# Optimization experiments

Measured on AMD Instinct MI355X. Metric: run time of the kernel, lower is better.

## Reference

```python
import jax, jax.numpy as jnp
import numpy as np

N = 50000   # nodes
E = 800000  # edges
G = 256     # graphs in batch
NF, EF, H, L = 16, 8, 128, 4
EPS = 1e-5


def setup_inputs() -> dict:
    key = jax.random.key(0)
    ks = jax.random.split(key, 20)
    s = 0.05
    return {
        "x": jax.random.normal(ks[0], (N, NF), jnp.float32),
        "edge_index": jax.random.randint(ks[1], (2, E), 0, N, dtype=jnp.int32),
        "edge_attr": jax.random.uniform(ks[2], (E, EF), jnp.float32),
        "batch": jnp.sort(jax.random.randint(ks[3], (N,), 0, G, dtype=jnp.int32)),
        "W_emb": jax.random.normal(ks[4], (NF, H), jnp.float32) * s,
        "b_emb": jnp.zeros((H,), jnp.float32),
        "Wf": jax.random.normal(ks[5], (L, 2 * H + EF, H), jnp.float32) * s,
        "bf": jnp.zeros((L, H), jnp.float32),
        "Ws": jax.random.normal(ks[6], (L, 2 * H + EF, H), jnp.float32) * s,
        "bs": jnp.zeros((L, H), jnp.float32),
        "gamma": jnp.ones((L, H), jnp.float32),
        "beta": jnp.zeros((L, H), jnp.float32),
        "W1": jax.random.normal(ks[7], (H, 64), jnp.float32) * s,
        "b1": jnp.zeros((64,), jnp.float32),
        "W2": jax.random.normal(ks[8], (64, 32), jnp.float32) * s,
        "b2": jnp.zeros((32,), jnp.float32),
        "W_out": jax.random.normal(ks[9], (32, 1), jnp.float32) * s,
        "b_out": jnp.zeros((1,), jnp.float32),
    }


def reference(x, edge_index, edge_attr, batch, W_emb, b_emb, Wf, bf, Ws, bs,
              gamma, beta, W1, b1, W2, b2, W_out, b_out):
    src, dst = edge_index[0], edge_index[1]  # message j->i: x_j=h[src], x_i=h[dst]
    h = jax.nn.relu(x @ W_emb + b_emb)       # [N, H]
    for l in range(L):
        # CGConv: z_ij = [x_i, x_j, e_ij]; gated message; sum-aggregate; +x residual
        z = jnp.concatenate([h[dst], h[src], edge_attr], axis=-1)  # [E, 2H+EF]
        m = jax.nn.sigmoid(z @ Wf[l] + bf[l]) * jax.nn.softplus(z @ Ws[l] + bs[l])
        agg = jax.ops.segment_sum(m, dst, num_segments=N)
        x_new = agg + h
        # BatchNorm1d (training-mode batch statistics, biased var)
        mu = x_new.mean(axis=0)
        var = x_new.var(axis=0)
        x_new = gamma[l] * (x_new - mu) * jax.lax.rsqrt(var + EPS) + beta[l]
        x_new = jax.nn.relu(x_new)
        h = h + x_new
    # global mean pool over graphs
    cnt = jax.ops.segment_sum(jnp.ones((N,), h.dtype), batch, num_segments=G)
    pooled = jax.ops.segment_sum(h, batch, num_segments=G) / jnp.maximum(cnt, 1.0)[:, None]
    g = jax.nn.relu(pooled @ W1 + b1)
    g = jax.nn.relu(g @ W2 + b2)
    return (g @ W_out + b_out).squeeze(-1)  # [G]
```

## Files before the change

### kernel.cpp

```cpp
#include <hip/hip_runtime.h>
#include <hip/hip_bf16.h>

#define H 128
#define EFD 8
#define NLAYER 4
#define ZDIM (2*H+EFD)

typedef float f32x2 __attribute__((ext_vector_type(2)));
typedef float f32x4 __attribute__((ext_vector_type(4)));
typedef short s16x8 __attribute__((ext_vector_type(8)));
typedef _Float16 f16x4 __attribute__((ext_vector_type(4)));
typedef unsigned int u32x2 __attribute__((ext_vector_type(2)));

#define PKFMA_LO(acc, a, b) asm("v_pk_fma_f32 %0, %1, %2, %0 op_sel:[0,0,0] op_sel_hi:[0,1,1]" : "+v"(acc) : "v"(a), "v"(b))
#define PKFMA_HI(acc, a, b) asm("v_pk_fma_f32 %0, %1, %2, %0 op_sel:[1,0,0] op_sel_hi:[1,1,1]" : "+v"(acc) : "v"(a), "v"(b))
#define PKFMA_LO_INIT(dst, a, b, c) asm("v_pk_fma_f32 %0, %1, %2, %3 op_sel:[0,0,0] op_sel_hi:[0,1,1]" : "=v"(dst) : "v"(a), "v"(b), "v"(c))
#define FMAMIX_LO(dst, h2, add) asm("v_fma_mix_f32 %0, %1, 1.0, %2 op_sel:[0,0,0] op_sel_hi:[1,0,0]" : "=v"(dst) : "v"(h2), "v"(add))
#define FMAMIX_HI(dst, h2, add) asm("v_fma_mix_f32 %0, %1, 1.0, %2 op_sel:[1,0,0] op_sel_hi:[1,0,0]" : "=v"(dst) : "v"(h2), "v"(add))

#define L2E 1.44269504088896340736f
#define LN2 0.69314718055994530942f

__device__ __forceinline__ unsigned short f2bf(float x){
    unsigned u = __float_as_uint(x);
    return (unsigned short)((u + 0x7FFFu + ((u>>16)&1u)) >> 16);
}

__global__ void embed_kernel(const float* __restrict__ x, const float* __restrict__ We,
                             const float* __restrict__ be, float* __restrict__ h, int N){
    int idx = blockIdx.x*blockDim.x + threadIdx.x;
    if (idx >= N*H) return;
    int n = idx >> 7, f = idx & 127;
    float a = be[f];
    #pragma unroll
    for (int k=0;k<16;k++) a = fmaf(x[n*16+k], We[k*H+f], a);
    h[idx] = fmaxf(a, 0.f);
}

__global__ void hist_kernel(const int* __restrict__ dstI, int* __restrict__ counts, int E){
    int e = blockIdx.x*blockDim.x + threadIdx.x;
    if (e < E) atomicAdd(&counts[dstI[e]], 1);
}

__global__ __launch_bounds__(1024) void scan1(const int* __restrict__ counts, int* __restrict__ incl,
                                              int* __restrict__ bsums, int N){
    __shared__ int lds[1024];
    int t = threadIdx.x;
    int i = blockIdx.x*1024 + t;
    int v = (i < N) ? counts[i] : 0;
    lds[t] = v;
    __syncthreads();
    for (int off=1; off<1024; off<<=1){
        int add = (t>=off) ? lds[t-off] : 0;
        __syncthreads();
        lds[t] += add;
        __syncthreads();
    }
    if (i < N) incl[i] = lds[t];
    if (t == 1023) bsums[blockIdx.x] = lds[1023];
}

__global__ __launch_bounds__(64) void scan2(int* bsums, int nb){
    int t = threadIdx.x;
    if (nb <= 64){
        int orig = (t < nb) ? bsums[t] : 0;
        int v = orig;
        for (int off=1; off<64; off<<=1){
            int n = __shfl_up(v, off);
            if (t >= off) v += n;
        }
        if (t < nb) bsums[t] = v - orig;
    } else if (t == 0){
        int run = 0;
        for (int b=0;b<nb;b++){ int v = bsums[b]; bsums[b] = run; run += v; }
    }
}

__global__ __launch_bounds__(1024) void scan3(const int* incl, const int* __restrict__ counts,
                                              const int* __restrict__ bsums, int* __restrict__ rowptr,
                                              int* cursor, int N, int E){
    int i = blockIdx.x*1024 + threadIdx.x;
    if (i >= N) return;
    int ex = incl[i] - counts[i] + bsums[blockIdx.x];
    rowptr[i] = ex;
    cursor[i] = ex;
    if (i == N-1) rowptr[N] = E;
}

__global__ void scatter_kernel(const int* __restrict__ srcI, const int* __restrict__ dstI,
                               const float* __restrict__ eattr, int* __restrict__ cursor,
                               int* __restrict__ src_s, float* __restrict__ ea_s, int E){
    int e = blockIdx.x*blockDim.x + threadIdx.x;
    if (e >= E) return;
    int d = dstI[e];
    int pos = atomicAdd(&cursor[d], 1);
    src_s[pos] = srcI[e];
    const float4* s4 = (const float4*)(eattr + (size_t)e*EFD);
    float4* o4 = (float4*)(ea_s + (size_t)pos*EFD);
    o4[0] = s4[0]; o4[1] = s4[1];
}

__global__ __launch_bounds__(256) void wpack_kernel(const float* __restrict__ Wf, const float* __restrict__ Ws,
        s16x8* __restrict__ bhi, s16x8* __restrict__ blo){
    int idx = blockIdx.x*256 + threadIdx.x;
    int l = idx & 63, ct = (idx>>6)&7, ks = (idx>>9)&3, w = (idx>>11)&3, layer = idx>>13;
    int cp = w*128 + ct*16 + (l&15);
    int k0 = ks*32 + ((l>>4)<<3);
    const float* WfL = Wf + (size_t)layer*ZDIM*H;
    const float* WsL = Ws + (size_t)layer*ZDIM*H;
    int colIn = cp & 127;
    int sel = cp >> 7;
    const float* Wm = (sel & 1) ? WsL : WfL;
    int krow = (sel >> 1) ? H : 0;
    s16x8 vh, vl;
    #pragma unroll
    for (int e=0;e<8;e++){
        float v = Wm[(size_t)(krow + k0 + e)*H + colIn];
        unsigned short hb = f2bf(v);
        float rem = v - __uint_as_float(((unsigned)hb)<<16);
        vh[e] = (short)hb;
        vl[e] = (short)f2bf(rem);
    }
    bhi[idx] = vh;
    blo[idx] = vl;
}

__global__ __launch_bounds__(512, 2) void table_mfma(
        float* __restrict__ h, const float* __restrict__ xn, const float* __restrict__ scsh,
        const s16x8* __restrict__ bhi, const s16x8* __restrict__ blo,
        const float* __restrict__ bf_l, const float* __restrict__ bs_l,
        float* __restrict__ TD, _Float16* __restrict__ TS16, int N, int layer, int ntiles){
    __shared__ __align__(16) short amat[2][32*136];
    const int t = threadIdx.x;
    const int lane = t & 63, W = t >> 6;
    const int ow = W >> 1, ctbase = (W & 1)*4;
    const int rbase = lane & 15, kg = lane >> 4;

    s16x8 Bh[4][4], Bl[4][4];
    {
        const size_t bbase = ((size_t)layer*4 + ow)*2048;
        #pragma unroll
        for (int ks=0;ks<4;ks++)
            #pragma unroll
            for (int c=0;c<4;c++){
                Bh[ks][c] = bhi[bbase + ks*512 + (ctbase+c)*64 + lane];
                Bl[ks][c] = blo[bbase + ks*512 + (ctbase+c)*64 + lane];
            }
        #pragma unroll
        for (int ks=0;ks<4;ks++)
            #pragma unroll
            for (int c=0;c<4;c++) asm volatile("" : "+v"(Bh[ks][c]), "+v"(Bl[ks][c]));
    }
    int c_local[4], off16[4];
    float bv[4];
    #pragma unroll
    for (int c=0;c<4;c++){
        c_local[c] = (ctbase+c)*16 + rbase;
        off16[c] = (c_local[c] >> 1)*4 + ((ow & 1) << 1) + (c_local[c] & 1);
        bv[c] = (ow == 0) ? bf_l[c_local[c]]*L2E : (ow == 1) ? bs_l[c_local[c]]*L2E : 0.f;
    }
    const int srow = t >> 4;
    const int kb = (t & 15)*8;
    float sc8[8], sh8[8];
    if (scsh){
        #pragma unroll
        for (int q=0;q<8;q+=4){
            *(float4*)&sc8[q] = *(const float4*)(scsh + kb + q);
            *(float4*)&sh8[q] = *(const float4*)(scsh + H + kb + q);
        }
    }

    for (int tile = blockIdx.x; tile < ntiles; tile += gridDim.x){
        const int n0 = tile*32;
        {
            const int gn = n0 + srow;
            const bool valid = gn < N;
            float* hr = h + (size_t)gn*H + kb;
            float vv[8];
            if (scsh){
                const float* xr = xn + (size_t)gn*H + kb;
                #pragma unroll
                for (int q=0;q<8;q+=4){
                    float4 xv = valid ? *(const float4*)(xr + q) : make_float4(0.f,0.f,0.f,0.f);
                    float4 hv = valid ? *(const float4*)(hr + q) : make_float4(0.f,0.f,0.f,0.f);
                    vv[q]   = hv.x + fmaxf(fmaf(xv.x, sc8[q],   sh8[q]),   0.f);
                    vv[q+1] = hv.y + fmaxf(fmaf(xv.y, sc8[q+1], sh8[q+1]), 0.f);
                    vv[q+2] = hv.z + fmaxf(fmaf(xv.z, sc8[q+2], sh8[q+2]), 0.f);
                    vv[q+3] = hv.w + fmaxf(fmaf(xv.w, sc8[q+3], sh8[q+3]), 0.f);
                }
                if (valid){
                    #pragma unroll
                    for (int q=0;q<8;q+=4){
                        float4 o; o.x=vv[q]; o.y=vv[q+1]; o.z=vv[q+2]; o.w=vv[q+3];
                        *(float4*)(hr + q) = o;
                    }
                }
            } else {
                #pragma unroll
                for (int q=0;q<8;q+=4){
                    float4 hv = valid ? *(const float4*)(hr + q) : make_float4(0.f,0.f,0.f,0.f);
                    vv[q]=hv.x; vv[q+1]=hv.y; vv[q+2]=hv.z; vv[q+3]=hv.w;
                }
            }
            s16x8 hv2, lv2;
            #pragma unroll
            for (int q=0;q<8;q++){
                unsigned short hb = f2bf(vv[q]);
                float rem = vv[q] - __uint_as_float(((unsigned)hb)<<16);
                hv2[q] = (short)hb;
                lv2[q] = (short)f2bf(rem);
            }
            *(s16x8*)&amat[0][srow*136 + kb] = hv2;
            *(s16x8*)&amat[1][srow*136 + kb] = lv2;
        }
        __syncthreads();
        f32x4 acc[2][4];
        #pragma unroll
        for (int rt=0;rt<2;rt++)
            #pragma unroll
            for (int c=0;c<4;c++){ acc[rt][c][0]=0.f; acc[rt][c][1]=0.f; acc[rt][c][2]=0.f; acc[rt][c][3]=0.f; }
        #pragma unroll
        for (int ks=0;ks<4;ks++){
            s16x8 ah[2], al[2];
            #pragma unroll
            for (int rt=0;rt<2;rt++){
                const int ao = (rbase + 16*rt)*136 + ks*32 + kg*8;
                ah[rt] = *(const s16x8*)&amat[0][ao];
                al[rt] = *(const s16x8*)&amat[1][ao];
            }
            #pragma unroll
            for (int c=0;c<4;c++)
                #pragma unroll
                for (int rt=0;rt<2;rt++){
                    acc[rt][c] = __builtin_amdgcn_mfma_f32_16x16x32_bf16(ah[rt], Bh[ks][c], acc[rt][c], 0, 0, 0);
                    acc[rt][c] = __builtin_amdgcn_mfma_f32_16x16x32_bf16(ah[rt], Bl[ks][c], acc[rt][c], 0, 0, 0);
                    acc[rt][c] = __builtin_amdgcn_mfma_f32_16x16x32_bf16(al[rt], Bh[ks][c], acc[rt][c], 0, 0, 0);
                }
        }
        if (ow < 2){
            const int colbase = (ow & 1)*128;
            #pragma unroll
            for (int c=0;c<4;c++)
                #pragma unroll
                for (int rt=0;rt<2;rt++){
                    const int nrow0 = n0 + 16*rt + kg*4;
                    #pragma unroll
                    for (int r=0;r<4;r++){
                        const int nd = nrow0 + r;
                        if (nd < N) TD[(size_t)nd*256 + colbase + c_local[c]] = fmaf(acc[rt][c][r], L2E, bv[c]);
                    }
                }
        } else {
            #pragma unroll
            for (int c=0;c<4;c++)
                #pragma unroll
                for (int rt=0;rt<2;rt++){
                    const int nrow0 = n0 + 16*rt + kg*4;
                    #pragma unroll
                    for (int r=0;r<4;r++){
                        const int nd = nrow0 + r;
                        if (nd < N) TS16[(size_t)nd*256 + off16[c]] = (_Float16)(acc[rt][c][r]*L2E);
                    }
                }
        }
        __syncthreads();
    }
}

__global__ __launch_bounds__(256, 4) void agg_kernel(
        const float* __restrict__ TD, const _Float16* __restrict__ TS16,
        const int* __restrict__ rowptr, const int* __restrict__ src_s, const float* __restrict__ ea_s,
        const float* __restrict__ Wf_l, const float* __restrict__ Ws_l,
        const float* __restrict__ h, float* __restrict__ xn, int N){
    __shared__ float wE[2048];
    const int t = threadIdx.x;
    {
        const float4* a = (const float4*)(Wf_l + 2*H*H);
        const float4* b = (const float4*)(Ws_l + 2*H*H);
        float4 va = a[t], vb = b[t];
        va.x*=L2E; va.y*=L2E; va.z*=L2E; va.w*=L2E;
        vb.x*=L2E; vb.y*=L2E; vb.z*=L2E; vb.w*=L2E;
        ((float4*)wE)[t] = va;
        ((float4*)wE)[256 + t] = vb;
    }
    __syncthreads();
    const int k = t & 63;
    const int i = blockIdx.x*4 + (t >> 6);
    if (i >= N) return;
    f32x2 wef2[8], wes2[8];
    #pragma unroll
    for (int r=0;r<8;r++){
        wef2[r] = *(const f32x2*)&wE[r*128 + 2*k];
        wes2[r] = *(const f32x2*)&wE[1024 + r*128 + 2*k];
    }
    #pragma unroll
    for (int r=0;r<8;r++) asm volatile("" : "+v"(wef2[r]), "+v"(wes2[r]));
    const f32x2* td = (const f32x2*)(TD + ((size_t)i << 8));
    f32x2 fd2 = td[k], sd2 = td[64+k];
    f32x2 acc = {0.f, 0.f};
    const int e0 = __builtin_amdgcn_readfirstlane(rowptr[i]);
    const int e1 = __builtin_amdgcn_readfirstlane(rowptr[i+1]);
    const int myoff = 4*k;
    const int last = e1 - 1;

    auto JID = [&](int e)->int {
        int ec = (e <= last) ? e : last;
        return __builtin_amdgcn_readfirstlane(src_s[ec]);
    };
    auto GATHER = [&](int j)->f16x4 {
        return *(const f16x4*)(TS16 + (((size_t)(unsigned)j) << 8) + myoff);
    };
    auto BODY = [&](int e, f16x4 tv){
        const float* ep = ea_s + (size_t)e*EFD;
        f32x4 eaA = *(const f32x4*)(ep);
        f32x4 eaB = *(const f32x4*)(ep + 4);
        f32x2 ea0 = __builtin_shufflevector(eaA, eaA, 0, 1);
        f32x2 ea1 = __builtin_shufflevector(eaA, eaA, 2, 3);
        f32x2 ea2 = __builtin_shufflevector(eaB, eaB, 0, 1);
        f32x2 ea3 = __builtin_shufflevector(eaB, eaB, 2, 3);
        f32x2 ef, es;
        PKFMA_LO_INIT(ef, ea0, wef2[0], fd2);
        PKFMA_HI(ef, ea0, wef2[1]);
        PKFMA_LO(ef, ea1, wef2[2]); PKFMA_HI(ef, ea1, wef2[3]);
        PKFMA_LO(ef, ea2, wef2[4]); PKFMA_HI(ef, ea2, wef2[5]);
        PKFMA_LO(ef, ea3, wef2[6]); PKFMA_HI(ef, ea3, wef2[7]);
        PKFMA_LO_INIT(es, ea0, wes2[0], sd2);
        PKFMA_HI(es, ea0, wes2[1]);
        PKFMA_LO(es, ea1, wes2[2]); PKFMA_HI(es, ea1, wes2[3]);
        PKFMA_LO(es, ea2, wes2[4]); PKFMA_HI(es, ea2, wes2[5]);
        PKFMA_LO(es, ea3, wes2[6]); PKFMA_HI(es, ea3, wes2[7]);
        u32x2 tu = *(u32x2*)&tv;
        float gx, gy, px, py;
        FMAMIX_LO(gx, tu.x, ef.x);
        FMAMIX_HI(gy, tu.x, ef.y);
        FMAMIX_LO(px, tu.y, es.x);
        FMAMIX_HI(py, tu.y, es.y);
        float sx = __builtin_amdgcn_rcpf(1.0f + __builtin_amdgcn_exp2f(-gx));
        float sy = __builtin_amdgcn_rcpf(1.0f + __builtin_amdgcn_exp2f(-gy));
        float tx = fmaxf(px, 0.f) + __builtin_amdgcn_logf(1.0f + __builtin_amdgcn_exp2f(-fabsf(px)));
        float ty = fmaxf(py, 0.f) + __builtin_amdgcn_logf(1.0f + __builtin_amdgcn_exp2f(-fabsf(py)));
        acc.x = fmaf(sx*tx, LN2, acc.x);
        acc.y = fmaf(sy*ty, LN2, acc.y);
    };

    if (e0 < e1){
        int j0 = JID(e0);
        int j1 = JID(e0+1);
        f16x4 tvA = GATHER(j0);
        f16x4 tvB = GATHER(j1);
        int jA = JID(e0+2);
        int jB = JID(e0+3);
        int e = e0;
        for (; e + 1 < e1; e += 2){
            int jA2 = JID(e+4);
            BODY(e, tvA);
            tvA = GATHER(jA);
            int jB2 = JID(e+5);
            BODY(e+1, tvB);
            tvB = GATHER(jB);
            jA = jA2; jB = jB2;
        }
        if (e < e1) BODY(e, tvA);
    }
    f32x2 hv = *(const f32x2*)(h + ((size_t)i << 7) + 2*k);
    f32x2 o = acc + hv;
    *(f32x2*)(xn + ((size_t)i << 7) + 2*k) = o;
}

__global__ __launch_bounds__(256) void stats_kernel(const float* __restrict__ xn, double* __restrict__ sums, int N){
    __shared__ double l1[128], l2[128];
    const int f = threadIdx.x & 127;
    const int half = threadIdx.x >> 7;
    const int nb = gridDim.x;
    const int per = (N + nb - 1)/nb;
    const int r0 = blockIdx.x*per;
    const int r1 = min(N, r0+per);
    double s = 0.0, s2 = 0.0;
    for (int r=r0+half; r<r1; r+=2){
        float v = xn[(size_t)r*H + f];
        s += v; s2 += (double)v*(double)v;
    }
    if (half == 1){ l1[f] = s; l2[f] = s2; }
    __syncthreads();
    if (half == 0){
        s += l1[f]; s2 += l2[f];
        atomicAdd(&sums[f], s);
        atomicAdd(&sums[H+f], s2);
    }
}

__global__ void finalize_bn(double* __restrict__ sums, const float* __restrict__ gamma_l,
                            const float* __restrict__ beta_l, float* __restrict__ scsh, int N){
    int f = threadIdx.x;
    if (f >= H) return;
    double mu = sums[f]/(double)N;
    double var = sums[H+f]/(double)N - mu*mu;
    if (var < 0.0) var = 0.0;
    float sc = (float)((double)gamma_l[f] / sqrt(var + 1e-5));
    scsh[f]   = sc;
    scsh[H+f] = (float)((double)beta_l[f] - mu*(double)sc);
    sums[f] = 0.0;
    sums[H+f] = 0.0;
}

__global__ __launch_bounds__(128) void pool_mlp_kernel(const float* __restrict__ h, const float* __restrict__ xn,
        const float* __restrict__ scsh, const int* __restrict__ batch,
        const float* __restrict__ W1, const float* __restrict__ b1,
        const float* __restrict__ W2, const float* __restrict__ b2,
        const float* __restrict__ Wo, const float* __restrict__ bo,
        float* __restrict__ out, int N){
    __shared__ float row[128];
    __shared__ float g1[64];
    __shared__ float g2[32];
    const int g = blockIdx.x;
    const int t = threadIdx.x;
    int lo = 0, hi = N;
    while (lo < hi){ int m = (lo+hi)>>1; if (batch[m] < g) lo = m+1; else hi = m; }
    const int s0 = lo;
    hi = N;
    while (lo < hi){ int m = (lo+hi)>>1; if (batch[m] < g+1) lo = m+1; else hi = m; }
    const int s1 = lo;
    const float sc = scsh[t], sh = scsh[H+t];
    float acc = 0.f;
    for (int r = s0; r < s1; ++r){
        float hv = h[(size_t)r*H + t];
        float xv = xn[(size_t)r*H + t];
        acc += hv + fmaxf(fmaf(xv, sc, sh), 0.f);
    }
    const float inv = 1.0f/fmaxf((float)(s1-s0), 1.0f);
    row[t] = acc*inv;
    __syncthreads();
    if (t < 64){
        float a = b1[t];
        #pragma unroll 4
        for (int i2=0;i2<128;i2++) a = fmaf(row[i2], W1[i2*64+t], a);
        g1[t] = fmaxf(a, 0.f);
    }
    __syncthreads();
    if (t < 32){
        float b = b2[t];
        #pragma unroll 4
        for (int i2=0;i2<64;i2++) b = fmaf(g1[i2], W2[i2*32+t], b);
        g2[t] = fmaxf(b, 0.f);
    }
    __syncthreads();
    if (t < 64){
        float p = (t < 32) ? g2[t]*Wo[t] : 0.f;
        for (int off=32; off>0; off>>=1) p += __shfl_down(p, off);
        if (t == 0) out[g] = p + bo[0];
    }
}

extern "C" void kernel_launch(void* const* d_in, const int* in_sizes, int n_in,
                              void* d_out, int out_size, void* d_ws, size_t ws_size,
                              hipStream_t stream){
    const float* x     = (const float*)d_in[0];
    const int*   eidx  = (const int*)d_in[1];
    const float* eattr = (const float*)d_in[2];
    const int*   batch = (const int*)d_in[3];
    const float* W_emb = (const float*)d_in[4];
    const float* b_emb = (const float*)d_in[5];
    const float* Wf    = (const float*)d_in[6];
    const float* bf    = (const float*)d_in[7];
    const float* Wsm   = (const float*)d_in[8];
    const float* bs    = (const float*)d_in[9];
    const float* gamma = (const float*)d_in[10];
    const float* beta  = (const float*)d_in[11];
    const float* W1    = (const float*)d_in[12];
    const float* b1    = (const float*)d_in[13];
    const float* W2    = (const float*)d_in[14];
    const float* b2    = (const float*)d_in[15];
    const float* Wo    = (const float*)d_in[16];
    const float* bo    = (const float*)d_in[17];
    float* out = (float*)d_out;

    const int N = in_sizes[0]/16;
    const int E = in_sizes[1]/2;
    const int G = out_size;

    const int* srcI = eidx;
    const int* dstI = eidx + E;

    char* p = (char*)d_ws;
    auto alloc = [&](size_t bytes)->char*{ char* r = p; p += (bytes + 255) & ~255ull; return r; };
    float*     h      = (float*)     alloc((size_t)N*H*4);
    float*     xn     = (float*)     alloc((size_t)N*H*4);
    float*     TD     = (float*)     alloc((size_t)N*2*H*4);
    _Float16*  TS16   = (_Float16*)  alloc((size_t)N*2*H*2);
    float*     ea_s   = (float*)     alloc((size_t)E*EFD*4);
    int*       src_s  = (int*)       alloc((size_t)E*4);
    int*       rowptr = (int*)       alloc((size_t)(N+1)*4);
    int*       cursor = (int*)       alloc((size_t)N*4);
    int*       counts = (int*)       alloc((size_t)N*4);
    int*       bsums  = (int*)       alloc(256*4);
    double*    sums   = (double*)    alloc(2*H*8);
    float*     scsh   = (float*)     alloc(2*H*4);
    s16x8*     bhi    = (s16x8*)     alloc((size_t)NLAYER*8192*16);
    s16x8*     blo    = (s16x8*)     alloc((size_t)NLAYER*8192*16);

    const int thr = 256;
    hipMemsetAsync(counts, 0, (size_t)N*4, stream);
    hipMemsetAsync(sums, 0, 2*H*8, stream);
    embed_kernel<<<(N*H + thr-1)/thr, thr, 0, stream>>>(x, W_emb, b_emb, h, N);
    hist_kernel<<<(E + thr-1)/thr, thr, 0, stream>>>(dstI, counts, E);
    int nb = (N + 1023)/1024;
    scan1<<<nb, 1024, 0, stream>>>(counts, cursor, bsums, N);
    scan2<<<1, 64, 0, stream>>>(bsums, nb);
    scan3<<<nb, 1024, 0, stream>>>(cursor, counts, bsums, rowptr, cursor, N, E);
    scatter_kernel<<<(E + thr-1)/thr, thr, 0, stream>>>(srcI, dstI, eattr, cursor, src_s, ea_s, E);
    wpack_kernel<<<128, 256, 0, stream>>>(Wf, Wsm, bhi, blo);

    const int ntiles = (N + 31)/32;
    for (int l=0;l<NLAYER;l++){
        table_mfma<<<256, 512, 0, stream>>>(h, xn, (l==0)?nullptr:scsh, bhi, blo,
                                            bf + l*H, bs + l*H, TD, TS16, N, l, ntiles);
        agg_kernel<<<(N+3)/4, 256, 0, stream>>>(TD, TS16, rowptr, src_s, ea_s,
                                                Wf + (size_t)l*ZDIM*H, Wsm + (size_t)l*ZDIM*H, h, xn, N);
        stats_kernel<<<256, 256, 0, stream>>>(xn, sums, N);
        finalize_bn<<<1, 128, 0, stream>>>(sums, gamma + l*H, beta + l*H, scsh, N);
    }

    pool_mlp_kernel<<<G, 128, 0, stream>>>(h, xn, scsh, batch, W1, b1, W2, b2, Wo, bo, out, N);
}
```

Measured before the change: 848.5 us.

## Merge dst/src tables into one fp16 row, stage outputs through LDS

The per-node destination table (previously fp32) and the source table (fp16) are combined into a single 512-half row per node, with the dst part also stored in fp16. table_mfma now writes MFMA results into a padded LDS tile and then emits coalesced 16-byte row stores, replacing scattered 2/4-byte global stores. This reduces table write traffic and store transaction count, and halves the dst-table read in agg. The cost is fp16 precision on the dst pre-activations, an extra LDS round trip and barrier, and larger LDS use that may limit occupancy.

```diff
diff --git a/kernel.cpp b/kernel.cpp
--- a/kernel.cpp
+++ b/kernel.cpp
@@ -20,6 +20,7 @@
 
 #define L2E 1.44269504088896340736f
 #define LN2 0.69314718055994530942f
+#define OPITCH 520
 
 __device__ __forceinline__ unsigned short f2bf(float x){
     unsigned u = __float_as_uint(x);
@@ -129,8 +130,9 @@
         float* __restrict__ h, const float* __restrict__ xn, const float* __restrict__ scsh,
         const s16x8* __restrict__ bhi, const s16x8* __restrict__ blo,
         const float* __restrict__ bf_l, const float* __restrict__ bs_l,
-        float* __restrict__ TD, _Float16* __restrict__ TS16, int N, int layer, int ntiles){
+        _Float16* __restrict__ T16, int N, int layer, int ntiles){
     __shared__ __align__(16) short amat[2][32*136];
+    __shared__ __align__(16) _Float16 outs[32*OPITCH];
     const int t = threadIdx.x;
     const int lane = t & 63, W = t >> 6;
     const int ow = W >> 1, ctbase = (W & 1)*4;
@@ -151,13 +153,13 @@
             #pragma unroll
             for (int c=0;c<4;c++) asm volatile("" : "+v"(Bh[ks][c]), "+v"(Bl[ks][c]));
     }
-    int c_local[4], off16[4];
+    int offT[4];
     float bv[4];
     #pragma unroll
     for (int c=0;c<4;c++){
-        c_local[c] = (ctbase+c)*16 + rbase;
-        off16[c] = (c_local[c] >> 1)*4 + ((ow & 1) << 1) + (c_local[c] & 1);
-        bv[c] = (ow == 0) ? bf_l[c_local[c]]*L2E : (ow == 1) ? bs_l[c_local[c]]*L2E : 0.f;
+        const int cl = (ctbase+c)*16 + rbase;
+        offT[c] = (ow>>1)*256 + ((cl>>1)<<2) + ((ow&1)<<1) + (cl&1);
+        bv[c] = (ow == 0) ? bf_l[cl]*L2E : (ow == 1) ? bs_l[cl]*L2E : 0.f;
     }
     const int srow = t >> 4;
     const int kb = (t & 15)*8;
@@ -237,38 +239,34 @@
                     acc[rt][c] = __builtin_amdgcn_mfma_f32_16x16x32_bf16(al[rt], Bh[ks][c], acc[rt][c], 0, 0, 0);
                 }
         }
-        if (ow < 2){
-            const int colbase = (ow & 1)*128;
-            #pragma unroll
-            for (int c=0;c<4;c++)
+        #pragma unroll
+        for (int c=0;c<4;c++)
+            #pragma unroll
+            for (int rt=0;rt<2;rt++){
+                const int nrow = 16*rt + kg*4;
                 #pragma unroll
-                for (int rt=0;rt<2;rt++){
-                    const int nrow0 = n0 + 16*rt + kg*4;
-                    #pragma unroll
-                    for (int r=0;r<4;r++){
-                        const int nd = nrow0 + r;
-                        if (nd < N) TD[(size_t)nd*256 + colbase + c_local[c]] = fmaf(acc[rt][c][r], L2E, bv[c]);
-                    }
+                for (int r=0;r<4;r++)
+                    outs[(nrow + r)*OPITCH + offT[c]] = (_Float16)fmaf(acc[rt][c][r], L2E, bv[c]);
+            }
+        __syncthreads();
+        {
+            const int colb = (t & 63)*8;
+            #pragma unroll
+            for (int ps=0; ps<4; ps++){
+                const int row = ps*8 + W;
+                const int nd = n0 + row;
+                if (nd < N){
+                    uint4 v = *(const uint4*)&outs[row*OPITCH + colb];
+                    *(uint4*)(T16 + (size_t)nd*512 + colb) = v;
                 }
-        } else {
-            #pragma unroll
-            for (int c=0;c<4;c++)
-                #pragma unroll
-                for (int rt=0;rt<2;rt++){
-                    const int nrow0 = n0 + 16*rt + kg*4;
-                    #pragma unroll
-                    for (int r=0;r<4;r++){
-                        const int nd = nrow0 + r;
-                        if (nd < N) TS16[(size_t)nd*256 + off16[c]] = (_Float16)(acc[rt][c][r]*L2E);
-                    }
-                }
+            }
         }
         __syncthreads();
     }
 }
 
 __global__ __launch_bounds__(256, 4) void agg_kernel(
-        const float* __restrict__ TD, const _Float16* __restrict__ TS16,
+        const _Float16* __restrict__ T16,
         const int* __restrict__ rowptr, const int* __restrict__ src_s, const float* __restrict__ ea_s,
         const float* __restrict__ Wf_l, const float* __restrict__ Ws_l,
         const float* __restrict__ h, float* __restrict__ xn, int N){
@@ -295,8 +293,10 @@
     }
     #pragma unroll
     for (int r=0;r<8;r++) asm volatile("" : "+v"(wef2[r]), "+v"(wes2[r]));
-    const f32x2* td = (const f32x2*)(TD + ((size_t)i << 8));
-    f32x2 fd2 = td[k], sd2 = td[64+k];
+    f16x4 dv = *(const f16x4*)(T16 + ((size_t)i << 9) + 4*k);
+    f32x2 fd2, sd2;
+    fd2.x = (float)dv[0]; fd2.y = (float)dv[1];
+    sd2.x = (float)dv[2]; sd2.y = (float)dv[3];
     f32x2 acc = {0.f, 0.f};
     const int e0 = __builtin_amdgcn_readfirstlane(rowptr[i]);
     const int e1 = __builtin_amdgcn_readfirstlane(rowptr[i+1]);
@@ -308,7 +308,7 @@
         return __builtin_amdgcn_readfirstlane(src_s[ec]);
     };
     auto GATHER = [&](int j)->f16x4 {
-        return *(const f16x4*)(TS16 + (((size_t)(unsigned)j) << 8) + myoff);
+        return *(const f16x4*)(T16 + 256 + (((size_t)(unsigned)j) << 9) + myoff);
     };
     auto BODY = [&](int e, f16x4 tv){
         const float* ep = ea_s + (size_t)e*EFD;
@@ -485,8 +485,7 @@
     auto alloc = [&](size_t bytes)->char*{ char* r = p; p += (bytes + 255) & ~255ull; return r; };
     float*     h      = (float*)     alloc((size_t)N*H*4);
     float*     xn     = (float*)     alloc((size_t)N*H*4);
-    float*     TD     = (float*)     alloc((size_t)N*2*H*4);
-    _Float16*  TS16   = (_Float16*)  alloc((size_t)N*2*H*2);
+    _Float16*  T16    = (_Float16*)  alloc((size_t)N*512*2);
     float*     ea_s   = (float*)     alloc((size_t)E*EFD*4);
     int*       src_s  = (int*)       alloc((size_t)E*4);
     int*       rowptr = (int*)       alloc((size_t)(N+1)*4);
@@ -513,8 +512,8 @@
     const int ntiles = (N + 31)/32;
     for (int l=0;l<NLAYER;l++){
         table_mfma<<<256, 512, 0, stream>>>(h, xn, (l==0)?nullptr:scsh, bhi, blo,
-                                            bf + l*H, bs + l*H, TD, TS16, N, l, ntiles);
-        agg_kernel<<<(N+3)/4, 256, 0, stream>>>(TD, TS16, rowptr, src_s, ea_s,
+                                            bf + l*H, bs + l*H, T16, N, l, ntiles);
+        agg_kernel<<<(N+3)/4, 256, 0, stream>>>(T16, rowptr, src_s, ea_s,
                                                 Wf + (size_t)l*ZDIM*H, Wsm + (size_t)l*ZDIM*H, h, xn, N);
         stats_kernel<<<256, 256, 0, stream>>>(xn, sums, N);
         finalize_bn<<<1, 128, 0, stream>>>(sums, gamma + l*H, beta + l*H, scsh, N);
```

Measured after the change: 832.5 us. Within noise of the previous version (-1.9%).
